# Kernel tuning notes

Hardware: AMD Instinct MI355X
Metric: run time of the kernel (lower is better)

The kernel has to match this reference:

```python
import jax, jax.numpy as jnp
import numpy as np

N, E = 100000, 1600000
IN, ED, H, HL, OUT = 32, 8, 16, 64, 4
BN_EPS = 1e-5


def setup_inputs() -> dict:
    key = jax.random.key(0)
    keys = iter(jax.random.split(key, 64))

    def rn(*s):
        return jax.random.normal(next(keys), s, jnp.float32) * 0.1

    inp = {}
    inp["x"] = jax.random.normal(next(keys), (N, IN), jnp.float32)
    inp["edge_index"] = jax.random.randint(next(keys), (2, E), 0, N)
    inp["edge_attr"] = jax.random.normal(next(keys), (E, ED), jnp.float32)
    for c, din in ((1, IN), (2, H), (3, H)):
        inp[f"ew{c}"] = rn(ED, din)   # GINEConv edge lin: edge_dim -> in_channels
        inp[f"eb{c}"] = rn(din)
        inp[f"wa{c}"] = rn(din, H)    # nn Linear 1
        inp[f"ba{c}"] = rn(H)
        inp[f"g{c}"] = jnp.ones((H,), jnp.float32)    # BN gamma
        inp[f"be{c}"] = jnp.zeros((H,), jnp.float32)  # BN beta
        inp[f"m{c}"] = rn(H)                           # BN running mean
        inp[f"v{c}"] = jax.random.uniform(next(keys), (H,), jnp.float32, 0.5, 1.5)  # BN running var
        inp[f"wb{c}"] = rn(H, H)      # nn Linear 2
        inp[f"bb{c}"] = rn(H)
    inp["lw1"] = rn(3 * H, HL)
    inp["lb1"] = rn(HL)
    inp["lw2"] = rn(HL, OUT)
    inp["lb2"] = rn(OUT)
    return inp


def gine_conv(x, edge_attr, src, dst, ew, eb, wa, ba, g, be, m, v, wb, bb):
    # message: relu(x_j + lin_edge(edge_attr)); aggregate: sum at dst; eps = 0
    e = edge_attr @ ew + eb                      # [E, din]
    msg = jax.nn.relu(x[src] + e)                # [E, din]
    agg = jax.ops.segment_sum(msg, dst, num_segments=x.shape[0])  # [N, din]
    h = (x + agg) @ wa + ba                      # Linear 1
    h = (h - m) * jax.lax.rsqrt(v + BN_EPS) * g + be  # BatchNorm1d (eval)
    h = jax.nn.relu(h)
    h = jax.nn.relu(h @ wb + bb)                 # Linear 2 + ReLU
    return h


def reference(x, edge_index, edge_attr,
              ew1, eb1, wa1, ba1, g1, be1, m1, v1, wb1, bb1,
              ew2, eb2, wa2, ba2, g2, be2, m2, v2, wb2, bb2,
              ew3, eb3, wa3, ba3, g3, be3, m3, v3, wb3, bb3,
              lw1, lb1, lw2, lb2):
    src, dst = edge_index[0], edge_index[1]
    h1 = gine_conv(x, edge_attr, src, dst, ew1, eb1, wa1, ba1, g1, be1, m1, v1, wb1, bb1)
    h2 = gine_conv(h1, edge_attr, src, dst, ew2, eb2, wa2, ba2, g2, be2, m2, v2, wb2, bb2)
    h3 = gine_conv(h2, edge_attr, src, dst, ew3, eb3, wa3, ba3, g3, be3, m3, v3, wb3, bb3)
    h = jnp.concatenate((h1, h2, h3), axis=1)    # [N, 3H]
    h = jax.nn.relu(h @ lw1 + lb1)               # dropout p=0.5 is identity in eval
    return h @ lw2 + lb2                         # [N, OUT]
```

## Files before the change

### kernel.cpp

```cpp
#include <hip/hip_runtime.h>
#include <hip/hip_bf16.h>

#define BN_EPS 1e-5f
#define BINSHIFT 6
#define BINW 64
#define NBLK 256


__global__ __launch_bounds__(256)
void hist2d_kernel(const int* __restrict__ dst, int* __restrict__ histmat,
                   int E, int nbins, int chunk) {
    __shared__ int h[2048];
    for (int i = threadIdx.x; i < nbins; i += 256) h[i] = 0;
    __syncthreads();
    int b = blockIdx.x;
    int e0 = b * chunk;
    int e1 = min(E, e0 + chunk);
    for (int e = e0 + threadIdx.x; e < e1; e += 256)
        atomicAdd(&h[dst[e] >> BINSHIFT], 1);
    __syncthreads();
    int* row = histmat + (size_t)b * nbins;
    for (int i = threadIdx.x; i < nbins; i += 256) row[i] = h[i];
}

__global__ __launch_bounds__(256)
void colsum_kernel(const int* __restrict__ histmat, int* __restrict__ bincnt,
                   int nbins) {
    int bin = blockIdx.x * 256 + threadIdx.x;
    if (bin >= nbins) return;
    int s = 0;
    for (int r = 0; r < NBLK; ++r) s += histmat[(size_t)r * nbins + bin];
    bincnt[bin] = s;
}

__global__ __launch_bounds__(1024)
void bin_scan_kernel(const int* __restrict__ bincnt, int* __restrict__ binstart,
                     int nbins, int E) {
    __shared__ int a[2048];
    __shared__ int b[1024];
    int t = threadIdx.x;
    a[t]        = (t < nbins) ? bincnt[t] : 0;
    a[t + 1024] = (t + 1024 < nbins) ? bincnt[t + 1024] : 0;
    __syncthreads();
    b[t] = a[2 * t] + a[2 * t + 1];
    __syncthreads();
    for (int off = 1; off < 1024; off <<= 1) {
        int v = (t >= off) ? b[t - off] : 0;
        __syncthreads();
        b[t] += v;
        __syncthreads();
    }
    int base = (t == 0) ? 0 : b[t - 1];
    if (2 * t < nbins)     binstart[2 * t]     = base;
    if (2 * t + 1 < nbins) binstart[2 * t + 1] = base + a[2 * t];
    if (t == 0) binstart[nbins] = E;
}

__global__ __launch_bounds__(256)
void rowscan_kernel(int* __restrict__ histmat, const int* __restrict__ binstart,
                    int nbins) {
    __shared__ int a[NBLK];
    int b = blockIdx.x;
    int t = threadIdx.x;
    int v = histmat[(size_t)t * nbins + b];
    a[t] = v;
    __syncthreads();
    for (int off = 1; off < NBLK; off <<= 1) {
        int add = (t >= off) ? a[t - off] : 0;
        __syncthreads();
        a[t] += add;
        __syncthreads();
    }
    histmat[(size_t)t * nbins + b] = binstart[b] + a[t] - v;
}

__global__ __launch_bounds__(256)
void place_kernel(const int* __restrict__ src, const int* __restrict__ dst,
                  const int* __restrict__ histmat, int2* __restrict__ tmp_meta,
                  int E, int nbins, int chunk) {
    __shared__ int cur[2048];
    int b = blockIdx.x;
    const int* row = histmat + (size_t)b * nbins;
    for (int i = threadIdx.x; i < nbins; i += 256) cur[i] = row[i];
    __syncthreads();
    int e0 = b * chunk;
    int e1 = min(E, e0 + chunk);
    for (int e = e0 + threadIdx.x; e < e1; e += 256) {
        int d = dst[e];
        int bin = d >> BINSHIFT;
        int pos = atomicAdd(&cur[bin], 1);
        int2 m;
        m.x = ((d & (BINW - 1)) << 20) | src[e];
        m.y = e;
        tmp_meta[pos] = m;
    }
}

__global__ __launch_bounds__(256)
void pass2_kernel(const int* __restrict__ binstart, const int2* __restrict__ tmp_meta,
                  const float* __restrict__ edge_attr,
                  int* __restrict__ rowstart, int* __restrict__ src_sorted,
                  float* __restrict__ ea_sorted, int N, int E, int nbins) {
    __shared__ int s_cur[BINW];
    int b = blockIdx.x;
    int node0 = b << BINSHIFT;
    int e0 = binstart[b], e1 = binstart[b + 1];
    int t = threadIdx.x;

    if (t < BINW) s_cur[t] = 0;
    __syncthreads();

    for (int e = e0 + t; e < e1; e += 256)
        atomicAdd(&s_cur[tmp_meta[e].x >> 20], 1);
    __syncthreads();

    if (t < BINW) {
        int val = s_cur[t];
        int inc = val;
#pragma unroll
        for (int off = 1; off < 64; off <<= 1) {
            int n = __shfl_up(inc, off);
            if (t >= off) inc += n;
        }
        int excl = e0 + inc - val;
        s_cur[t] = excl;
        int node = node0 + t;
        if (node <= N) rowstart[node] = excl;
    }
    __syncthreads();

    for (int e = e0 + t; e < e1; e += 256) {
        int2 m = tmp_meta[e];
        int dl   = m.x >> 20;
        int srcv = m.x & 0xFFFFF;
        int eid  = m.y;
        int fpos = atomicAdd(&s_cur[dl], 1);
        src_sorted[fpos] = srcv;
        const float4* sp = (const float4*)(edge_attr + (size_t)eid * 8);
        float4 a0 = sp[0], a1 = sp[1];
        float4* dp = (float4*)(ea_sorted + (size_t)fpos * 8);
        dp[0] = a0;
        dp[1] = a1;
    }
}

template<int DIN, int C, int S>
__global__ __launch_bounds__(256)
void gine_layer_wave(const float* __restrict__ xin,
                     const int*   __restrict__ rowstart,
                     const int*   __restrict__ src_sorted,
                     const float* __restrict__ ea_sorted,
                     const float* __restrict__ ew, const float* __restrict__ eb,
                     const float* __restrict__ wa, const float* __restrict__ ba,
                     const float* __restrict__ g, const float* __restrict__ be,
                     const float* __restrict__ m, const float* __restrict__ v,
                     const float* __restrict__ wb, const float* __restrict__ bb,
                     float* __restrict__ hout,
                     int N) {
    static_assert(C * S == 64 && C * 4 == DIN, "lane layout");
    constexpr int PAD = DIN + 1;

    __shared__ float s_wa[DIN * 16];
    __shared__ float s_wb[256];
    __shared__ float s_ba[16], s_scale[16], s_shift[16], s_bb[16];
    __shared__ float s_s[16 * PAD];
    __shared__ float s_h[16 * 17];

    int t = threadIdx.x;
    for (int idx = t; idx < DIN * 16; idx += 256) s_wa[idx] = wa[idx];
    s_wb[t] = wb[t];
    if (t < 16) {
        s_ba[t] = ba[t];
        float sc = g[t] * rsqrtf(v[t] + BN_EPS);
        s_scale[t] = sc;
        s_shift[t] = be[t] - m[t] * sc;
        s_bb[t] = bb[t];
    }

    int w    = t >> 6;
    int lane = t & 63;
    int c    = lane / S;
    int s    = lane % S;
    int c0   = c * 4;

    float ew_r[8][4];
#pragma unroll
    for (int k = 0; k < 8; ++k) {
        float4 wv = *(const float4*)(ew + k * DIN + c0);
        ew_r[k][0] = wv.x; ew_r[k][1] = wv.y; ew_r[k][2] = wv.z; ew_r[k][3] = wv.w;
    }
    float4 ebv = *(const float4*)(eb + c0);
    float eb_r[4] = {ebv.x, ebv.y, ebv.z, ebv.w};

    int node0 = blockIdx.x * 16;

#pragma unroll
    for (int q = 0; q < 4; ++q) {
        int nl = w * 4 + q;
        int i  = node0 + nl;
        float acc[4] = {0.f, 0.f, 0.f, 0.f};
        if (i < N) {
            int e0 = rowstart[i];
            int e1 = rowstart[i + 1];
            for (int e = e0 + s; e < e1; e += S) {
                int sv = src_sorted[e];
                const float4* ep = (const float4*)(ea_sorted + (size_t)e * 8);
                float4 a0 = ep[0], a1 = ep[1];
                float4 xv = *(const float4*)(xin + (size_t)sv * DIN + c0);
                float av[8] = {a0.x, a0.y, a0.z, a0.w, a1.x, a1.y, a1.z, a1.w};
                float xr[4] = {xv.x, xv.y, xv.z, xv.w};
#pragma unroll
                for (int j = 0; j < 4; ++j) {
                    float lin = eb_r[j];
#pragma unroll
                    for (int k = 0; k < 8; ++k) lin = fmaf(av[k], ew_r[k][j], lin);
                    lin += xr[j];
                    acc[j] += (lin > 0.f ? lin : 0.f);
                }
            }
        }
#pragma unroll
        for (int mask = S >> 1; mask >= 1; mask >>= 1) {
#pragma unroll
            for (int j = 0; j < 4; ++j) acc[j] += __shfl_xor(acc[j], mask);
        }
        if (s == 0 && i < N) {
            float4 xi = *(const float4*)(xin + (size_t)i * DIN + c0);
            s_s[nl * PAD + c0 + 0] = acc[0] + xi.x;
            s_s[nl * PAD + c0 + 1] = acc[1] + xi.y;
            s_s[nl * PAD + c0 + 2] = acc[2] + xi.z;
            s_s[nl * PAD + c0 + 3] = acc[3] + xi.w;
        }
    }
    __syncthreads();

    int nl2 = t >> 4;
    int j   = t & 15;
    float a = s_ba[j];
#pragma unroll
    for (int k = 0; k < DIN; ++k)
        a = fmaf(s_s[nl2 * PAD + k], s_wa[k * 16 + j], a);
    a = a * s_scale[j] + s_shift[j];
    s_h[nl2 * 17 + j] = a > 0.f ? a : 0.f;
    __syncthreads();

    float o = s_bb[j];
#pragma unroll
    for (int k = 0; k < 16; ++k)
        o = fmaf(s_h[nl2 * 17 + k], s_wb[k * 16 + j], o);
    o = o > 0.f ? o : 0.f;
    int i2 = node0 + nl2;
    if (i2 < N) hout[(size_t)i2 * 16 + j] = o;
}

__global__ __launch_bounds__(256)
void final_kernel(const float* __restrict__ h1, const float* __restrict__ h2,
                  const float* __restrict__ h3,
                  const float* __restrict__ lw1, const float* __restrict__ lb1,
                  const float* __restrict__ lw2, const float* __restrict__ lb2,
                  float* __restrict__ out, int N) {
    constexpr int NPB = 64;
    __shared__ float s_lw1[48 * 64];
    __shared__ float s_lw2[64 * 4];
    __shared__ float s_lb1[64];
    __shared__ float s_lb2[4];
    __shared__ float s_c[NPB][49];

    int t = threadIdx.x;
    for (int idx = t; idx < 48 * 64; idx += 256) s_lw1[idx] = lw1[idx];
    s_lw2[t] = lw2[t];
    if (t < 64) s_lb1[t] = lb1[t];
    if (t < 4) s_lb2[t] = lb2[t];

    int nl = t >> 2;
    int l  = t & 3;
    int i  = blockIdx.x * NPB + nl;

    if (i < N) {
        float4 c1 = ((const float4*)(h1 + (size_t)i * 16))[l];
        float4 c2 = ((const float4*)(h2 + (size_t)i * 16))[l];
        float4 c3 = ((const float4*)(h3 + (size_t)i * 16))[l];
        s_c[nl][l * 4 + 0] = c1.x; s_c[nl][l * 4 + 1] = c1.y;
        s_c[nl][l * 4 + 2] = c1.z; s_c[nl][l * 4 + 3] = c1.w;
        s_c[nl][16 + l * 4 + 0] = c2.x; s_c[nl][16 + l * 4 + 1] = c2.y;
        s_c[nl][16 + l * 4 + 2] = c2.z; s_c[nl][16 + l * 4 + 3] = c2.w;
        s_c[nl][32 + l * 4 + 0] = c3.x; s_c[nl][32 + l * 4 + 1] = c3.y;
        s_c[nl][32 + l * 4 + 2] = c3.z; s_c[nl][32 + l * 4 + 3] = c3.w;
    }
    __syncthreads();

    float o0 = 0.f, o1 = 0.f, o2 = 0.f, o3 = 0.f;
    if (i < N) {
#pragma unroll 4
        for (int jj = 0; jj < 16; ++jj) {
            int j = l * 16 + jj;
            float a = s_lb1[j];
#pragma unroll
            for (int k = 0; k < 48; ++k) a = fmaf(s_c[nl][k], s_lw1[k * 64 + j], a);
            a = a > 0.f ? a : 0.f;
            o0 = fmaf(a, s_lw2[j * 4 + 0], o0);
            o1 = fmaf(a, s_lw2[j * 4 + 1], o1);
            o2 = fmaf(a, s_lw2[j * 4 + 2], o2);
            o3 = fmaf(a, s_lw2[j * 4 + 3], o3);
        }
    }
    o0 += __shfl_xor(o0, 1); o0 += __shfl_xor(o0, 2);
    o1 += __shfl_xor(o1, 1); o1 += __shfl_xor(o1, 2);
    o2 += __shfl_xor(o2, 1); o2 += __shfl_xor(o2, 2);
    o3 += __shfl_xor(o3, 1); o3 += __shfl_xor(o3, 2);
    if (i < N && l == 0) {
        float4 o = {o0 + s_lb2[0], o1 + s_lb2[1], o2 + s_lb2[2], o3 + s_lb2[3]};
        *(float4*)(out + (size_t)i * 4) = o;
    }
}

extern "C" void kernel_launch(void* const* d_in, const int* in_sizes, int n_in,
                              void* d_out, int out_size, void* d_ws, size_t ws_size,
                              hipStream_t stream) {
    const float* x  = (const float*)d_in[0];
    const int*   ei = (const int*)d_in[1];
    const float* ea = (const float*)d_in[2];
    const int N = in_sizes[0] / 32;
    const int E = in_sizes[1] / 2;
    const int* srci = ei;
    const int* dsti = ei + E;

    const float* lw1 = (const float*)d_in[33];
    const float* lb1 = (const float*)d_in[34];
    const float* lw2 = (const float*)d_in[35];
    const float* lb2 = (const float*)d_in[36];

    const int nbins = (N + BINW - 1) >> BINSHIFT;
    const int chunk = (E + NBLK - 1) / NBLK;

    char* p = (char*)d_ws;
    int*   binstart   = (int*)p;   p += (size_t)(nbins + 1 + 3) / 4 * 16;
    int*   bincnt     = (int*)p;   p += (size_t)(nbins + 3) / 4 * 16;
    int*   rowstart   = (int*)p;   p += (size_t)(N + 1 + 3) / 4 * 16;
    int*   histmat    = (int*)p;   p += (size_t)NBLK * nbins * 4;
    int*   src_sorted = (int*)p;   p += (size_t)E * 4;
    float* ea_sorted  = (float*)p; p += (size_t)E * 8 * 4;
    char*  u          = p;
    int2*  tmp_meta   = (int2*)u;
    float* h1         = (float*)u;
    float* h2         = h1 + (size_t)N * 16;
    float* h3         = h2 + (size_t)N * 16;

    hist2d_kernel<<<NBLK, 256, 0, stream>>>(dsti, histmat, E, nbins, chunk);
    colsum_kernel<<<(nbins + 255) / 256, 256, 0, stream>>>(histmat, bincnt, nbins);
    bin_scan_kernel<<<1, 1024, 0, stream>>>(bincnt, binstart, nbins, E);
    rowscan_kernel<<<nbins, NBLK, 0, stream>>>(histmat, binstart, nbins);
    place_kernel<<<NBLK, 256, 0, stream>>>(srci, dsti, histmat, tmp_meta,
                                           E, nbins, chunk);
    pass2_kernel<<<nbins, 256, 0, stream>>>(binstart, tmp_meta, ea,
                                            rowstart, src_sorted, ea_sorted,
                                            N, E, nbins);

    const int lblocks = (N + 15) / 16;
    gine_layer_wave<32, 8, 8><<<lblocks, 256, 0, stream>>>(
        x, rowstart, src_sorted, ea_sorted,
        (const float*)d_in[3], (const float*)d_in[4],
        (const float*)d_in[5], (const float*)d_in[6],
        (const float*)d_in[7], (const float*)d_in[8],
        (const float*)d_in[9], (const float*)d_in[10],
        (const float*)d_in[11], (const float*)d_in[12], h1, N);

    gine_layer_wave<16, 4, 16><<<lblocks, 256, 0, stream>>>(
        h1, rowstart, src_sorted, ea_sorted,
        (const float*)d_in[13], (const float*)d_in[14],
        (const float*)d_in[15], (const float*)d_in[16],
        (const float*)d_in[17], (const float*)d_in[18],
        (const float*)d_in[19], (const float*)d_in[20],
        (const float*)d_in[21], (const float*)d_in[22], h2, N);

    gine_layer_wave<16, 4, 16><<<lblocks, 256, 0, stream>>>(
        h2, rowstart, src_sorted, ea_sorted,
        (const float*)d_in[23], (const float*)d_in[24],
        (const float*)d_in[25], (const float*)d_in[26],
        (const float*)d_in[27], (const float*)d_in[28],
        (const float*)d_in[29], (const float*)d_in[30],
        (const float*)d_in[31], (const float*)d_in[32], h3, N);

    final_kernel<<<(N + 63) / 64, 256, 0, stream>>>(
        h1, h2, h3, lw1, lb1, lw2, lb2, (float*)d_out, N);
}
```

Baseline: 503.4 us.

## Scatter edge attributes during binning and prefetch next source index in aggregation

The place kernel now copies each edge's 8 attributes into a bin-ordered temporary buffer along with the packed metadata. Pass2 then reads attributes from that local bin region instead of gathering them randomly from the original array by edge id. The aggregation loop also software-prefetches the next src index so the dependent x gather can start sooner. The cost is an extra full write and read of the edge-attribute array through the temporary buffer, which now shares workspace with the h buffers.

```diff
diff --git a/kernel.cpp b/kernel.cpp
--- a/kernel.cpp
+++ b/kernel.cpp
@@ -76,7 +76,9 @@
 
 __global__ __launch_bounds__(256)
 void place_kernel(const int* __restrict__ src, const int* __restrict__ dst,
-                  const int* __restrict__ histmat, int2* __restrict__ tmp_meta,
+                  const float* __restrict__ edge_attr,
+                  const int* __restrict__ histmat,
+                  int* __restrict__ tmp_meta, float* __restrict__ tmp_ea,
                   int E, int nbins, int chunk) {
     __shared__ int cur[2048];
     int b = blockIdx.x;
@@ -89,18 +91,20 @@
         int d = dst[e];
         int bin = d >> BINSHIFT;
         int pos = atomicAdd(&cur[bin], 1);
-        int2 m;
-        m.x = ((d & (BINW - 1)) << 20) | src[e];
-        m.y = e;
-        tmp_meta[pos] = m;
-    }
-}
-
-__global__ __launch_bounds__(256)
-void pass2_kernel(const int* __restrict__ binstart, const int2* __restrict__ tmp_meta,
-                  const float* __restrict__ edge_attr,
+        tmp_meta[pos] = ((d & (BINW - 1)) << 20) | src[e];
+        const float4* sp = (const float4*)(edge_attr + (size_t)e * 8);
+        float4 a0 = sp[0], a1 = sp[1];
+        float4* dp = (float4*)(tmp_ea + (size_t)pos * 8);
+        dp[0] = a0;
+        dp[1] = a1;
+    }
+}
+
+__global__ __launch_bounds__(256)
+void pass2_kernel(const int* __restrict__ binstart, const int* __restrict__ tmp_meta,
+                  const float* __restrict__ tmp_ea,
                   int* __restrict__ rowstart, int* __restrict__ src_sorted,
-                  float* __restrict__ ea_sorted, int N, int E, int nbins) {
+                  float* __restrict__ ea_sorted, int N, int E) {
     __shared__ int s_cur[BINW];
     int b = blockIdx.x;
     int node0 = b << BINSHIFT;
@@ -111,7 +115,7 @@
     __syncthreads();
 
     for (int e = e0 + t; e < e1; e += 256)
-        atomicAdd(&s_cur[tmp_meta[e].x >> 20], 1);
+        atomicAdd(&s_cur[tmp_meta[e] >> 20], 1);
     __syncthreads();
 
     if (t < BINW) {
@@ -130,13 +134,12 @@
     __syncthreads();
 
     for (int e = e0 + t; e < e1; e += 256) {
-        int2 m = tmp_meta[e];
-        int dl   = m.x >> 20;
-        int srcv = m.x & 0xFFFFF;
-        int eid  = m.y;
+        int mx = tmp_meta[e];
+        int dl   = mx >> 20;
+        int srcv = mx & 0xFFFFF;
         int fpos = atomicAdd(&s_cur[dl], 1);
         src_sorted[fpos] = srcv;
-        const float4* sp = (const float4*)(edge_attr + (size_t)eid * 8);
+        const float4* sp = (const float4*)(tmp_ea + (size_t)e * 8);
         float4 a0 = sp[0], a1 = sp[1];
         float4* dp = (float4*)(ea_sorted + (size_t)fpos * 8);
         dp[0] = a0;
@@ -202,8 +205,11 @@
         if (i < N) {
             int e0 = rowstart[i];
             int e1 = rowstart[i + 1];
-            for (int e = e0 + s; e < e1; e += S) {
-                int sv = src_sorted[e];
+            int e  = e0 + s;
+            int sv = (e < e1) ? src_sorted[e] : 0;
+            for (; e < e1; e += S) {
+                int en = e + S;
+                int sv_next = (en < e1) ? src_sorted[en] : 0;
                 const float4* ep = (const float4*)(ea_sorted + (size_t)e * 8);
                 float4 a0 = ep[0], a1 = ep[1];
                 float4 xv = *(const float4*)(xin + (size_t)sv * DIN + c0);
@@ -217,6 +223,7 @@
                     lin += xr[j];
                     acc[j] += (lin > 0.f ? lin : 0.f);
                 }
+                sv = sv_next;
             }
         }
 #pragma unroll
@@ -341,7 +348,8 @@
     int*   src_sorted = (int*)p;   p += (size_t)E * 4;
     float* ea_sorted  = (float*)p; p += (size_t)E * 8 * 4;
     char*  u          = p;
-    int2*  tmp_meta   = (int2*)u;
+    int*   tmp_meta   = (int*)u;
+    float* tmp_ea     = (float*)(u + (size_t)E * 4);
     float* h1         = (float*)u;
     float* h2         = h1 + (size_t)N * 16;
     float* h3         = h2 + (size_t)N * 16;
@@ -350,11 +358,11 @@
     colsum_kernel<<<(nbins + 255) / 256, 256, 0, stream>>>(histmat, bincnt, nbins);
     bin_scan_kernel<<<1, 1024, 0, stream>>>(bincnt, binstart, nbins, E);
     rowscan_kernel<<<nbins, NBLK, 0, stream>>>(histmat, binstart, nbins);
-    place_kernel<<<NBLK, 256, 0, stream>>>(srci, dsti, histmat, tmp_meta,
-                                           E, nbins, chunk);
-    pass2_kernel<<<nbins, 256, 0, stream>>>(binstart, tmp_meta, ea,
+    place_kernel<<<NBLK, 256, 0, stream>>>(srci, dsti, ea, histmat,
+                                           tmp_meta, tmp_ea, E, nbins, chunk);
+    pass2_kernel<<<nbins, 256, 0, stream>>>(binstart, tmp_meta, tmp_ea,
                                             rowstart, src_sorted, ea_sorted,
-                                            N, E, nbins);
+                                            N, E);
 
     const int lblocks = (N + 15) / 16;
     gine_layer_wave<32, 8, 8><<<lblocks, 256, 0, stream>>>(
```

New measurement: 526.8 us. 4.7% more time.
